# Kernel tuning notes

Hardware: AMD Instinct MI355X
Metric: run time of the kernel (lower is better)

## Reference

```python
import jax, jax.numpy as jnp
import numpy as np

N = 50000        # n_nodes
E = 1_600_000    # n_edges (avg degree 32)
D = 128          # in_feat_dim
H = 128          # hidden_dim
OUT = 128        # out_feat_dim
EDGE_IN = 2 * D + 1 + 1  # h[row], h[col], dist_sq, edge_attr
act = jax.nn.silu


def _lin(k, fan_in, fan_out):
    lim = 1.0 / np.sqrt(fan_in)
    return jax.random.uniform(k, (fan_in, fan_out), jnp.float32, -lim, lim)


def setup_inputs() -> dict:
    key = jax.random.key(0)
    ks = jax.random.split(key, 24)
    inp = {
        "h": jax.random.normal(ks[0], (N, D), jnp.float32),
        "x": jax.random.normal(ks[1], (N, 3), jnp.float32),
        "edge_attr": jax.random.normal(ks[2], (E, 1), jnp.float32),
        "v_init": jax.random.normal(ks[3], (N, 3), jnp.float32),
        "edge_index": jax.random.randint(ks[4], (2, E), 0, N, jnp.int32),
        # edge_mlp: Linear(258,H), act, Linear(H,H), act
        "edge_W1": _lin(ks[5], EDGE_IN, H), "edge_b1": jnp.zeros((H,), jnp.float32),
        "edge_W2": _lin(ks[6], H, H), "edge_b2": jnp.zeros((H,), jnp.float32),
        # coord_mlp: Linear(H,H), act, Linear(H,1,bias=False)
        "coord_W1": _lin(ks[7], H, H), "coord_b1": jnp.zeros((H,), jnp.float32),
        "coord_W2": _lin(ks[8], H, 1),
        # infer_edge_step: Linear(H,H//2), act, Linear(H//2,1), sigmoid
        "inf_W1": _lin(ks[9], H, H // 2), "inf_b1": jnp.zeros((H // 2,), jnp.float32),
        "inf_W2": _lin(ks[10], H // 2, 1), "inf_b2": jnp.zeros((1,), jnp.float32),
        # node_mlp: Linear(D+H,H), act, Linear(H,OUT)
        "node_W1": _lin(ks[11], D + H, H), "node_b1": jnp.zeros((H,), jnp.float32),
        "node_W2": _lin(ks[12], H, OUT), "node_b2": jnp.zeros((OUT,), jnp.float32),
        # momentum_vel_mlp: Linear(D,H), act, Linear(H,1,bias=False)
        "vel_W1": _lin(ks[13], D, H), "vel_b1": jnp.zeros((H,), jnp.float32),
        "vel_W2": _lin(ks[14], H, 1),
    }
    return inp


def reference(h, x, edge_attr, v_init, edge_index,
              edge_W1, edge_b1, edge_W2, edge_b2,
              coord_W1, coord_b1, coord_W2,
              inf_W1, inf_b1, inf_W2, inf_b2,
              node_W1, node_b1, node_W2, node_b2,
              vel_W1, vel_b1, vel_W2):
    row, col = edge_index[0], edge_index[1]
    x_diff = x[row] - x[col]                                   # [E,3]
    dist_sq = jnp.sum(x_diff * x_diff, axis=1, keepdims=True)  # [E,1]
    ef = jnp.concatenate([h[row], h[col], dist_sq, edge_attr], axis=1)  # [E,258]
    m_ij = act(act(ef @ edge_W1 + edge_b1) @ edge_W2 + edge_b2)        # [E,H]
    e_ij = jax.nn.sigmoid(act(m_ij @ inf_W1 + inf_b1) @ inf_W2 + inf_b2)  # [E,1]
    phi_x = act(m_ij @ coord_W1 + coord_b1) @ coord_W2                 # [E,1]
    x_update = e_ij * (phi_x * x_diff)                                 # [E,3]
    m_ij = e_ij * m_ij

    vel_scale = act(h @ vel_W1 + vel_b1) @ vel_W2                      # [N,1]
    v_out = v_init * vel_scale                                         # [N,3]

    agg_x = jax.ops.segment_sum(x_update, row, num_segments=N)         # [N,3]
    m_i = jax.ops.segment_sum(m_ij, row, num_segments=N)               # [N,H]
    deg = jax.ops.segment_sum(jnp.ones((E,), jnp.float32), row, num_segments=N)
    has_edge = (deg > 0)[:, None]
    # nodes with no outgoing edges keep their original x (original loop skips them)
    x_out = jnp.where(has_edge, x + v_out + agg_x / (N - 1), x)

    node_in = jnp.concatenate([h, m_i], axis=1)                        # [N,D+H]
    h_out = act(node_in @ node_W1 + node_b1) @ node_W2 + node_b2       # [N,OUT]
    return (h_out, x_out, v_out)
```

## Files before the change

kernel.cpp:

```cpp
#include <hip/hip_runtime.h>
#include <hip/hip_bf16.h>

typedef __attribute__((ext_vector_type(8))) short short8;
typedef __attribute__((ext_vector_type(4))) float f32x4;
typedef __hip_bfloat16 bf16;

__device__ __forceinline__ short f2bs_rn(float f) {
    unsigned u = __builtin_bit_cast(unsigned, f);
    u += 0x7FFF + ((u >> 16) & 1);
    return (short)(u >> 16);
}
__device__ __forceinline__ float bs2f(short s) {
    unsigned u = ((unsigned)(unsigned short)s) << 16;
    return __builtin_bit_cast(float, u);
}
__device__ __forceinline__ float ldf(const void* p, int i, int flag) {
    return flag ? bs2f(((const short*)p)[i]) : ((const float*)p)[i];
}
__device__ __forceinline__ short ldbits(const void* p, int i, int flag) {
    return flag ? ((const short*)p)[i] : f2bs_rn(((const float*)p)[i]);
}
__device__ __forceinline__ void stf(void* p, int i, float v, int flag) {
    if (flag) ((bf16*)p)[i] = __float2bfloat16(v);
    else ((float*)p)[i] = v;
}
__device__ __forceinline__ float nz(float v) { return (v == v) ? v : 0.f; }
__device__ __forceinline__ float siluf(float v) {
    return v * __builtin_amdgcn_rcpf(1.f + __expf(-v));
}
__device__ __forceinline__ float sigmf(float v) {
    return __builtin_amdgcn_rcpf(1.f + __expf(-v));
}

__global__ void detect_kernel(const unsigned int* __restrict__ hw, int* __restrict__ flag) {
    unsigned int w = hw[threadIdx.x];
    unsigned int e = (w >> 7) & 0xFF;
    bool ok = (e >= 113 && e <= 135);
    unsigned long long m = __ballot(ok);
    if (threadIdx.x == 0) *flag = (__popcll(m) >= 32) ? 1 : 0;
}

__global__ void prep_kernel(
    const void* eW1, const void* eW2, const void* cW1, const void* iW1,
    const void* eb1, const void* eb2, const void* cb1, const void* cw2,
    const void* ib1, const void* iw2, const void* ib2, const void* nb1,
    const void* nb2, const void* vb1, const void* vW2,
    const void* nW1, const void* nW2, const void* vW1,
    short* __restrict__ W1t, short* __restrict__ W2t,
    short* __restrict__ cW1t, short* __restrict__ iW1t,
    float* __restrict__ biasblk, short* __restrict__ nW1b,
    short* __restrict__ nW2b, short* __restrict__ vW1b,
    const int* __restrict__ flagp) {
    const int flag = *flagp;
    int i = blockIdx.x * 256 + threadIdx.x;
    if (i < 36864) {
        int c = i >> 9, r = i & 511;
        int kc = c >> 3, nt = c & 7;
        int ln = r >> 3, j = r & 7;
        int k = kc * 32 + ((ln >> 4) << 3) + j;
        int n = nt * 16 + (ln & 15);
        W1t[i] = (k < 258) ? ldbits(eW1, k * 128 + n, flag) : (short)0;
        return;
    }
    i -= 36864;
    if (i < 16384) {
        int c = i >> 9, r = i & 511;
        int kc = c >> 3, nt = c & 7;
        int ln = r >> 3, j = r & 7;
        int k = kc * 32 + ((ln >> 4) << 3) + j;
        int n = nt * 16 + (ln & 15);
        W2t[i] = ldbits(eW2, k * 128 + n, flag);
        return;
    }
    i -= 16384;
    if (i < 16384) {
        int c = i >> 9, r = i & 511;
        int kc = c >> 3, nt = c & 7;
        int ln = r >> 3, j = r & 7;
        int k = kc * 32 + ((ln >> 4) << 3) + j;
        int n = nt * 16 + (ln & 15);
        cW1t[i] = ldbits(cW1, k * 128 + n, flag);
        return;
    }
    i -= 16384;
    if (i < 8192) {
        int c = i >> 9, r = i & 511;
        int kc = c >> 2, nt = c & 3;
        int ln = r >> 3, j = r & 7;
        int k = kc * 32 + ((ln >> 4) << 3) + j;
        int n = nt * 16 + (ln & 15);
        iW1t[i] = ldbits(iW1, k * 64 + n, flag);
        return;
    }
    i -= 8192;
    if (i < 1412) {
        float v;
        if (i < 128) v = ldf(eb1, i, flag);
        else if (i < 256) v = ldf(eb2, i - 128, flag);
        else if (i < 384) v = ldf(cb1, i - 256, flag);
        else if (i < 512) v = ldf(cw2, i - 384, flag);
        else if (i < 576) v = ldf(ib1, i - 512, flag);
        else if (i < 640) v = ldf(iw2, i - 576, flag);
        else if (i < 644) v = (i == 640) ? ldf(ib2, 0, flag) : 0.f;
        else if (i < 772) v = ldf(nb1, i - 644, flag);
        else if (i < 900) v = ldf(nb2, i - 772, flag);
        else if (i < 1028) v = ldf(vb1, i - 900, flag);
        else if (i < 1156) v = ldf(vW2, i - 1028, flag);
        else if (i < 1284) v = ldf(eW1, 256 * 128 + (i - 1156), flag);
        else v = ldf(eW1, 257 * 128 + (i - 1284), flag);
        biasblk[i] = v;
        return;
    }
    i -= 1412;
    if (i < 32768) {
        int c = i >> 9, r = i & 511;
        int kc = c >> 3, nt = c & 7;
        int ln = r >> 3, j = r & 7;
        int k = kc * 32 + ((ln >> 4) << 3) + j;
        int n = nt * 16 + (ln & 15);
        nW1b[i] = ldbits(nW1, k * 128 + n, flag);
        return;
    }
    i -= 32768;
    if (i < 16384) {
        int c = i >> 9, r = i & 511;
        int kc = c >> 3, nt = c & 7;
        int ln = r >> 3, j = r & 7;
        int k = kc * 32 + ((ln >> 4) << 3) + j;
        int n = nt * 16 + (ln & 15);
        nW2b[i] = ldbits(nW2, k * 128 + n, flag);
        return;
    }
    i -= 16384;
    if (i < 16384) {
        int c = i >> 9, r = i & 511;
        int kc = c >> 3, nt = c & 7;
        int ln = r >> 3, j = r & 7;
        int k = kc * 32 + ((ln >> 4) << 3) + j;
        int n = nt * 16 + (ln & 15);
        vW1b[i] = ldbits(vW1, k * 128 + n, flag);
    }
}

__global__ void convh_kernel(const void* __restrict__ h, short* __restrict__ hb,
                             const int* __restrict__ flagp, int n) {
    const int flag = *flagp;
    int i = blockIdx.x * 256 + threadIdx.x;
    if (i < n) hb[i] = ldbits(h, i, flag);
}

__global__ __launch_bounds__(256) void hw1_kernel(
    const short* __restrict__ hb, const short* __restrict__ W1t,
    short* __restrict__ hA, short* __restrict__ hB, int N) {
    const int tid = threadIdx.x;
    const int wv = tid >> 6;
    const int lane = tid & 63;
    const int n15 = lane & 15;
    const int quad = lane >> 4;
    const int base = blockIdx.x * 128 + wv * 32;

    f32x4 accA[2][8], accB[2][8];
#pragma unroll
    for (int m = 0; m < 2; ++m)
#pragma unroll
        for (int nt = 0; nt < 8; ++nt) {
            accA[m][nt] = (f32x4){0.f, 0.f, 0.f, 0.f};
            accB[m][nt] = (f32x4){0.f, 0.f, 0.f, 0.f};
        }

#pragma unroll
    for (int kc = 0; kc < 4; ++kc) {
        short8 a[2];
#pragma unroll
        for (int m = 0; m < 2; ++m) {
            int node = base + m * 16 + n15;
            if (node >= N) node = N - 1;
            a[m] = *(const short8*)(hb + node * 128 + kc * 32 + quad * 8);
        }
        const short* bpA = W1t + (kc * 8) * 512 + lane * 8;
        const short* bpB = W1t + ((kc + 4) * 8) * 512 + lane * 8;
#pragma unroll
        for (int nt = 0; nt < 8; ++nt) {
            short8 ba = *(const short8*)(bpA + nt * 512);
            short8 bb = *(const short8*)(bpB + nt * 512);
            accA[0][nt] = __builtin_amdgcn_mfma_f32_16x16x32_bf16(a[0], ba, accA[0][nt], 0, 0, 0);
            accA[1][nt] = __builtin_amdgcn_mfma_f32_16x16x32_bf16(a[1], ba, accA[1][nt], 0, 0, 0);
            accB[0][nt] = __builtin_amdgcn_mfma_f32_16x16x32_bf16(a[0], bb, accB[0][nt], 0, 0, 0);
            accB[1][nt] = __builtin_amdgcn_mfma_f32_16x16x32_bf16(a[1], bb, accB[1][nt], 0, 0, 0);
        }
    }

#pragma unroll
    for (int m = 0; m < 2; ++m)
#pragma unroll
        for (int nt = 0; nt < 8; ++nt)
#pragma unroll
            for (int r = 0; r < 4; ++r) {
                int node = base + m * 16 + quad * 4 + r;
                if (node < N) {
                    hA[node * 128 + nt * 16 + n15] = f2bs_rn(accA[m][nt][r]);
                    hB[node * 128 + nt * 16 + n15] = f2bs_rn(accB[m][nt][r]);
                }
            }
}

__global__ void count_kernel(const int* __restrict__ erow, int* __restrict__ cnt, int E) {
    int i = blockIdx.x * 256 + threadIdx.x;
    if (i < E) atomicAdd(&cnt[erow[i]], 1);
}

__global__ __launch_bounds__(1024) void scan1_kernel(const int* __restrict__ cnt,
                                                     int* __restrict__ off,
                                                     int* __restrict__ bsum, int N) {
    __shared__ int sm[1024];
    int t = threadIdx.x, i = blockIdx.x * 1024 + t;
    int c = (i < N) ? cnt[i] : 0;
    sm[t] = c;
    __syncthreads();
    for (int d = 1; d < 1024; d <<= 1) {
        int v = (t >= d) ? sm[t - d] : 0;
        __syncthreads();
        sm[t] += v;
        __syncthreads();
    }
    if (i < N) off[i] = sm[t] - c;
    if (t == 1023) bsum[blockIdx.x] = sm[1023];
}
__global__ void scan2_kernel(const int* __restrict__ bsum, int* __restrict__ bpre, int nb) {
    if (threadIdx.x == 0) {
        int run = 0;
        for (int b = 0; b < nb; ++b) { bpre[b] = run; run += bsum[b]; }
    }
}
__global__ void scan3_kernel(int* __restrict__ off, const int* __restrict__ bpre, int N) {
    int i = blockIdx.x * 256 + threadIdx.x;
    if (i < N) off[i] += bpre[i >> 10];
}
__global__ void fill_kernel(const int* __restrict__ erow, const int* __restrict__ off,
                            int* __restrict__ cur, int* __restrict__ elist, int E) {
    int i = blockIdx.x * 256 + threadIdx.x;
    if (i < E) {
        int r = erow[i];
        int p = off[r] + atomicAdd(&cur[r], 1);
        elist[p] = i;
    }
}

template <bool CSR>
__global__ __launch_bounds__(256, 6) void edge_kernel(
    const short* __restrict__ hA, const short* __restrict__ hB,
    const void* __restrict__ x, const void* __restrict__ eattr,
    const int* __restrict__ erow, const int* __restrict__ ecol,
    const int* __restrict__ elist,
    const short* __restrict__ W2f, const short* __restrict__ cW1f,
    const short* __restrict__ iW1f,
    const float* __restrict__ biasblk,
    float* __restrict__ m_i, float* __restrict__ agg_x, int E,
    const int* __restrict__ flagp) {
    const int flag = *flagp;
    __shared__ __align__(16) short tiles[4][16 * 136];
    const float* b1f = biasblk;
    const float* b2f = biasblk + 128;
    const float* cb1f = biasblk + 256;
    const float* cw2f = biasblk + 384;
    const float* ib1f = biasblk + 512;
    const float* iw2f = biasblk + 576;
    const float ib2s = biasblk[640];
    const float* w1df = biasblk + 1156;
    const float* w1af = biasblk + 1284;

    int bid;
    {
        const int nwg = gridDim.x;
        const int qq = nwg >> 3, r8 = nwg & 7;
        const int xcd = blockIdx.x & 7, idx = blockIdx.x >> 3;
        const int base = (xcd < r8) ? xcd * (qq + 1) : r8 * (qq + 1) + (xcd - r8) * qq;
        bid = base + idx;
    }

    const int tid = threadIdx.x;
    const int wv = tid >> 6;
    const int lane = tid & 63;
    const int n15 = lane & 15;
    const int quad = lane >> 4;
    const int wb = bid * 64 + wv * 16;

    int row_e, col_e;
    float dist, attr;
    {
        int slot = wb + n15;
        int sL = (slot < E) ? slot : (E - 1);
        int eL = CSR ? elist[sL] : sL;
        row_e = erow[eL];
        col_e = ecol[eL];
        float d = 0.f;
#pragma unroll
        for (int dd = 0; dd < 3; ++dd) {
            float xd = ldf(x, row_e * 3 + dd, flag) - ldf(x, col_e * 3 + dd, flag);
            d += xd * xd;
        }
        dist = d;
        attr = ldf(eattr, eL, flag);
    }

    short8 cB[4];
#pragma unroll
    for (int c = 0; c < 4; ++c)
        cB[c] = *(const short8*)(hB + col_e * 128 + c * 32 + quad * 8);

    short* tl = tiles[wv];
    short8 h1[4];
#pragma unroll
    for (int c = 0; c < 4; ++c) {
        short8 ra = *(const short8*)(hA + row_e * 128 + c * 32 + quad * 8);
        short8 ov;
#pragma unroll
        for (int j = 0; j < 8; ++j) {
            int f = c * 32 + quad * 8 + j;
            float v = bs2f(ra[j]) + bs2f(cB[c][j])
                    + dist * w1df[f] + attr * w1af[f] + b1f[f];
            ov[j] = f2bs_rn(siluf(v));
        }
        h1[c] = ov;
    }

    f32x4 acc2[8];
#pragma unroll
    for (int nt = 0; nt < 8; ++nt) acc2[nt] = (f32x4){0.f, 0.f, 0.f, 0.f};
#pragma unroll
    for (int kc = 0; kc < 4; ++kc) {
        short8 a = h1[kc];
        const short* bp = W2f + (kc * 8) * 512 + lane * 8;
#pragma unroll
        for (int nt = 0; nt < 8; ++nt) {
            short8 b = *(const short8*)(bp + nt * 512);
            acc2[nt] = __builtin_amdgcn_mfma_f32_16x16x32_bf16(a, b, acc2[nt], 0, 0, 0);
        }
    }

#pragma unroll
    for (int nt = 0; nt < 8; ++nt) {
        float bv = b2f[nt * 16 + n15];
#pragma unroll
        for (int r = 0; r < 4; ++r)
            tl[(quad * 4 + r) * 136 + nt * 16 + n15] = f2bs_rn(siluf(acc2[nt][r] + bv));
    }

    f32x4 acc4[4];
#pragma unroll
    for (int nt = 0; nt < 4; ++nt) acc4[nt] = (f32x4){0.f, 0.f, 0.f, 0.f};
#pragma unroll
    for (int kc = 0; kc < 4; ++kc) {
        short8 a = *(const short8*)(tl + n15 * 136 + kc * 32 + quad * 8);
        const short* bp = iW1f + (kc * 4) * 512 + lane * 8;
#pragma unroll
        for (int nt = 0; nt < 4; ++nt) {
            short8 b = *(const short8*)(bp + nt * 512);
            acc4[nt] = __builtin_amdgcn_mfma_f32_16x16x32_bf16(a, b, acc4[nt], 0, 0, 0);
        }
    }
    float eij[4];
    {
        float inp[4] = {0.f, 0.f, 0.f, 0.f};
#pragma unroll
        for (int nt = 0; nt < 4; ++nt) {
            float ib = ib1f[nt * 16 + n15];
            float iw = iw2f[nt * 16 + n15];
#pragma unroll
            for (int r = 0; r < 4; ++r) inp[r] += siluf(acc4[nt][r] + ib) * iw;
        }
#pragma unroll
        for (int mk = 1; mk < 16; mk <<= 1)
#pragma unroll
            for (int r = 0; r < 4; ++r) inp[r] += __shfl_xor(inp[r], mk);
#pragma unroll
        for (int r = 0; r < 4; ++r) eij[r] = sigmf(inp[r] + ib2s);
    }

    f32x4 acc3[8];
#pragma unroll
    for (int nt = 0; nt < 8; ++nt) acc3[nt] = (f32x4){0.f, 0.f, 0.f, 0.f};
#pragma unroll
    for (int kc = 0; kc < 4; ++kc) {
        short8 a = *(const short8*)(tl + n15 * 136 + kc * 32 + quad * 8);
        const short* bp = cW1f + (kc * 8) * 512 + lane * 8;
#pragma unroll
        for (int nt = 0; nt < 8; ++nt) {
            short8 b = *(const short8*)(bp + nt * 512);
            acc3[nt] = __builtin_amdgcn_mfma_f32_16x16x32_bf16(a, b, acc3[nt], 0, 0, 0);
        }
    }

    {
        float php[4] = {0.f, 0.f, 0.f, 0.f};
#pragma unroll
        for (int nt = 0; nt < 8; ++nt) {
            float cb = cb1f[nt * 16 + n15];
            float cw = cw2f[nt * 16 + n15];
#pragma unroll
            for (int r = 0; r < 4; ++r) php[r] += siluf(acc3[nt][r] + cb) * cw;
        }
#pragma unroll
        for (int mk = 1; mk < 16; mk <<= 1)
#pragma unroll
            for (int r = 0; r < 4; ++r) php[r] += __shfl_xor(php[r], mk);

        float sv[4];
#pragma unroll
        for (int r = 0; r < 4; ++r) sv[r] = eij[r] * php[r];
        const int srcl = (n15 >> 2) * 16;
        float t0 = __shfl(sv[0], srcl);
        float t1 = __shfl(sv[1], srcl);
        float t2 = __shfl(sv[2], srcl);
        float t3 = __shfl(sv[3], srcl);
        const int rr = n15 & 3;
        float s_e = (rr == 0) ? t0 : (rr == 1) ? t1 : (rr == 2) ? t2 : t3;

        float val = 0.f;
        if (quad < 3) {
            float xd = ldf(x, row_e * 3 + quad, flag) - ldf(x, col_e * 3 + quad, flag);
            val = ((wb + n15) < E) ? nz(s_e * xd) : 0.f;
        }

        const int ebase = wb;
        if (CSR) {
            int p = 0;
            while (p < 16 && (ebase + p) < E) {
                int rowp = __shfl(row_e, p);
                unsigned bal = (unsigned)__ballot(row_e == rowp) & 0xFFFFu;
                unsigned bits = (~bal) >> p;
                int q = p + __builtin_ctz(bits);

                float av = (n15 >= p && n15 < q) ? val : 0.f;
#pragma unroll
                for (int mk = 1; mk < 16; mk <<= 1) av += __shfl_xor(av, mk);
                if (n15 == 0 && quad < 3) atomicAdd(&agg_x[rowp * 3 + quad], av);

                float s[8];
#pragma unroll
                for (int nt = 0; nt < 8; ++nt) s[nt] = 0.f;
#pragma unroll
                for (int r = 0; r < 4; ++r) {
                    int idx = quad * 4 + r;
                    bool in = (idx >= p) && (idx < q) && ((ebase + idx) < E);
                    float w = in ? eij[r] : 0.f;
#pragma unroll
                    for (int nt = 0; nt < 8; ++nt)
                        s[nt] += w * bs2f(tl[idx * 136 + nt * 16 + n15]);
                }
#pragma unroll
                for (int nt = 0; nt < 8; ++nt) {
                    s[nt] += __shfl_xor(s[nt], 16);
                    s[nt] += __shfl_xor(s[nt], 32);
                }
                if (quad == 0) {
#pragma unroll
                    for (int nt = 0; nt < 8; ++nt)
                        atomicAdd(&m_i[(size_t)rowp * 128 + nt * 16 + n15], nz(s[nt]));
                }
                p = q;
            }
        } else {
            if (quad < 3 && (wb + n15) < E)
                atomicAdd(&agg_x[row_e * 3 + quad], val);
#pragma unroll
            for (int nt = 0; nt < 8; ++nt)
#pragma unroll
                for (int r = 0; r < 4; ++r) {
                    int idx = quad * 4 + r;
                    if ((ebase + idx) < E) {
                        int er = __shfl(row_e, idx);
                        atomicAdd(&m_i[er * 128 + nt * 16 + n15],
                                  nz(eij[r] * bs2f(tl[idx * 136 + nt * 16 + n15])));
                    }
                }
        }
    }
}

__global__ __launch_bounds__(256, 4) void node_kernel(
    const short* __restrict__ hb, const void* __restrict__ x,
    const void* __restrict__ v_init,
    const int* __restrict__ cnt,
    const float* __restrict__ m_i, const float* __restrict__ agg_x,
    const short* __restrict__ nW1f, const short* __restrict__ nW2f,
    const short* __restrict__ vW1f, const float* __restrict__ biasblk,
    void* __restrict__ out, int N, int xbase, int vbase, float inv_nm1,
    const int* __restrict__ flagp) {
    const int flag = *flagp;
    __shared__ __align__(16) short tiles[4][16 * 136];
    const float* nb1f = biasblk + 644;
    const float* nb2f = biasblk + 772;
    const float* vb1f = biasblk + 900;
    const float* vW2f = biasblk + 1028;

    const int tid = threadIdx.x;
    const int wv = tid >> 6;
    const int lane = tid & 63;
    const int n15 = lane & 15;
    const int quad = lane >> 4;
    const int base = blockIdx.x * 64 + wv * 16;

    short* tl = tiles[wv];

    {
        int node = base + n15;
        if (node >= N) node = N - 1;
#pragma unroll
        for (int c = 0; c < 4; ++c) {
            const float* mp = m_i + (size_t)node * 128 + c * 32 + quad * 8;
            short8 ov;
#pragma unroll
            for (int j = 0; j < 8; ++j) ov[j] = f2bs_rn(nz(mp[j]));
            *(short8*)(tl + n15 * 136 + c * 32 + quad * 8) = ov;
        }
    }
    int anode = base + n15;
    if (anode >= N) anode = N - 1;

    f32x4 acc[8];
#pragma unroll
    for (int nt = 0; nt < 8; ++nt) acc[nt] = (f32x4){0.f, 0.f, 0.f, 0.f};
#pragma unroll
    for (int kc = 0; kc < 4; ++kc) {
        short8 a = *(const short8*)(hb + (size_t)anode * 128 + kc * 32 + quad * 8);
        const short* bp = vW1f + (kc * 8) * 512 + lane * 8;
#pragma unroll
        for (int nt = 0; nt < 8; ++nt) {
            short8 b = *(const short8*)(bp + nt * 512);
            acc[nt] = __builtin_amdgcn_mfma_f32_16x16x32_bf16(a, b, acc[nt], 0, 0, 0);
        }
    }
    float vsc[4] = {0.f, 0.f, 0.f, 0.f};
#pragma unroll
    for (int nt = 0; nt < 8; ++nt) {
        int j = nt * 16 + n15;
        float vb = vb1f[j];
        float vw = vW2f[j];
#pragma unroll
        for (int r = 0; r < 4; ++r) vsc[r] += siluf(acc[nt][r] + vb) * vw;
    }
#pragma unroll
    for (int mk = 1; mk < 16; mk <<= 1)
#pragma unroll
        for (int r = 0; r < 4; ++r) vsc[r] += __shfl_xor(vsc[r], mk);

#pragma unroll
    for (int nt = 0; nt < 8; ++nt) acc[nt] = (f32x4){0.f, 0.f, 0.f, 0.f};
#pragma unroll
    for (int kc = 0; kc < 8; ++kc) {
        short8 a;
        if (kc < 4) a = *(const short8*)(hb + (size_t)anode * 128 + kc * 32 + quad * 8);
        else        a = *(const short8*)(tl + n15 * 136 + (kc - 4) * 32 + quad * 8);
        const short* bp = nW1f + (kc * 8) * 512 + lane * 8;
#pragma unroll
        for (int nt = 0; nt < 8; ++nt) {
            short8 b = *(const short8*)(bp + nt * 512);
            acc[nt] = __builtin_amdgcn_mfma_f32_16x16x32_bf16(a, b, acc[nt], 0, 0, 0);
        }
    }
#pragma unroll
    for (int nt = 0; nt < 8; ++nt) {
        float bv = nb1f[nt * 16 + n15];
#pragma unroll
        for (int r = 0; r < 4; ++r)
            tl[(quad * 4 + r) * 136 + nt * 16 + n15] = f2bs_rn(siluf(acc[nt][r] + bv));
    }

#pragma unroll
    for (int nt = 0; nt < 8; ++nt) acc[nt] = (f32x4){0.f, 0.f, 0.f, 0.f};
#pragma unroll
    for (int kc = 0; kc < 4; ++kc) {
        short8 a = *(const short8*)(tl + n15 * 136 + kc * 32 + quad * 8);
        const short* bp = nW2f + (kc * 8) * 512 + lane * 8;
#pragma unroll
        for (int nt = 0; nt < 8; ++nt) {
            short8 b = *(const short8*)(bp + nt * 512);
            acc[nt] = __builtin_amdgcn_mfma_f32_16x16x32_bf16(a, b, acc[nt], 0, 0, 0);
        }
    }
#pragma unroll
    for (int nt = 0; nt < 8; ++nt) {
        float bv = nb2f[nt * 16 + n15];
#pragma unroll
        for (int r = 0; r < 4; ++r) {
            int node = base + quad * 4 + r;
            if (node < N) stf(out, node * 128 + nt * 16 + n15, nz(acc[nt][r] + bv), flag);
        }
    }

    if (n15 < 3) {
#pragma unroll
        for (int r = 0; r < 4; ++r) {
            int node = base + quad * 4 + r;
            if (node >= N) continue;
            int d = n15;
            float vj = nz(ldf(v_init, node * 3 + d, flag) * vsc[r]);
            stf(out, vbase + node * 3 + d, vj, flag);
            float xv = ldf(x, node * 3 + d, flag);
            float xo = (cnt[node] > 0) ? xv + vj + nz(agg_x[node * 3 + d]) * inv_nm1 : xv;
            stf(out, xbase + node * 3 + d, nz(xo), flag);
        }
    }
}

template <bool CSR>
__global__ __launch_bounds__(256, 2) void edge_kernel_old(
    const short* __restrict__ hb, const void* __restrict__ x,
    const void* __restrict__ eattr,
    const int* __restrict__ erow, const int* __restrict__ ecol,
    const int* __restrict__ elist,
    const short* __restrict__ W1f, const short* __restrict__ W2f,
    const short* __restrict__ cW1f, const short* __restrict__ iW1f,
    const float* __restrict__ biasblk,
    float* __restrict__ m_i, float* __restrict__ agg_x, int E,
    const int* __restrict__ flagp) {
    const int flag = *flagp;
    __shared__ __align__(16) short tiles[8][16 * 136];
    const float* b1f = biasblk;
    const float* b2f = biasblk + 128;
    const float* cb1f = biasblk + 256;
    const float* cw2f = biasblk + 384;
    const float* ib1f = biasblk + 512;
    const float* iw2f = biasblk + 576;
    const float ib2s = biasblk[640];

    const int tid = threadIdx.x;
    const int wv = tid >> 6;
    const int lane = tid & 63;
    const int n15 = lane & 15;
    const int quad = lane >> 4;
    const int wb = blockIdx.x * 128 + wv * 32;

    int row_e[2], col_e[2];
    float dist[2], attr[2];
#pragma unroll
    for (int m = 0; m < 2; ++m) {
        int slot = wb + m * 16 + n15;
        int sL = (slot < E) ? slot : (E - 1);
        int eL = CSR ? elist[sL] : sL;
        row_e[m] = erow[eL];
        col_e[m] = ecol[eL];
        float d = 0.f;
#pragma unroll
        for (int dd = 0; dd < 3; ++dd) {
            float xd = ldf(x, row_e[m] * 3 + dd, flag) - ldf(x, col_e[m] * 3 + dd, flag);
            d += xd * xd;
        }
        dist[m] = d;
        attr[m] = ldf(eattr, eL, flag);
    }

    short8 cA[2][4];
#pragma unroll
    for (int m = 0; m < 2; ++m)
#pragma unroll
        for (int c = 0; c < 4; ++c)
            cA[m][c] = *(const short8*)(hb + col_e[m] * 128 + c * 32 + quad * 8);

    f32x4 acc1[2][8];
#pragma unroll
    for (int m = 0; m < 2; ++m)
#pragma unroll
        for (int nt = 0; nt < 8; ++nt) acc1[m][nt] = (f32x4){0.f, 0.f, 0.f, 0.f};

#pragma unroll
    for (int kc = 0; kc < 9; ++kc) {
        short8 a[2];
        if (kc < 4) {
            a[0] = *(const short8*)(hb + row_e[0] * 128 + kc * 32 + quad * 8);
            a[1] = *(const short8*)(hb + row_e[1] * 128 + kc * 32 + quad * 8);
        } else if (kc < 8) {
            a[0] = cA[0][kc - 4];
            a[1] = cA[1][kc - 4];
        } else {
#pragma unroll
            for (int m = 0; m < 2; ++m) {
#pragma unroll
                for (int t = 0; t < 8; ++t) a[m][t] = 0;
                if (quad == 0) { a[m][0] = f2bs_rn(dist[m]); a[m][1] = f2bs_rn(attr[m]); }
            }
        }
        const short* bp = W1f + (kc * 8) * 512 + lane * 8;
#pragma unroll
        for (int nt = 0; nt < 8; ++nt) {
            short8 b = *(const short8*)(bp + nt * 512);
            acc1[0][nt] = __builtin_amdgcn_mfma_f32_16x16x32_bf16(a[0], b, acc1[0][nt], 0, 0, 0);
            acc1[1][nt] = __builtin_amdgcn_mfma_f32_16x16x32_bf16(a[1], b, acc1[1][nt], 0, 0, 0);
        }
    }

#pragma unroll
    for (int m = 0; m < 2; ++m) {
        short* tl = tiles[wv * 2 + m];
#pragma unroll
        for (int nt = 0; nt < 8; ++nt) {
            float bv = b1f[nt * 16 + n15];
#pragma unroll
            for (int r = 0; r < 4; ++r)
                tl[(quad * 4 + r) * 136 + nt * 16 + n15] = f2bs_rn(siluf(acc1[m][nt][r] + bv));
        }
    }

    f32x4 acc2[2][8];
#pragma unroll
    for (int m = 0; m < 2; ++m)
#pragma unroll
        for (int nt = 0; nt < 8; ++nt) acc2[m][nt] = (f32x4){0.f, 0.f, 0.f, 0.f};
#pragma unroll
    for (int kc = 0; kc < 4; ++kc) {
        short8 a[2];
#pragma unroll
        for (int m = 0; m < 2; ++m)
            a[m] = *(const short8*)(tiles[wv * 2 + m] + n15 * 136 + kc * 32 + quad * 8);
        const short* bp = W2f + (kc * 8) * 512 + lane * 8;
#pragma unroll
        for (int nt = 0; nt < 8; ++nt) {
            short8 b = *(const short8*)(bp + nt * 512);
            acc2[0][nt] = __builtin_amdgcn_mfma_f32_16x16x32_bf16(a[0], b, acc2[0][nt], 0, 0, 0);
            acc2[1][nt] = __builtin_amdgcn_mfma_f32_16x16x32_bf16(a[1], b, acc2[1][nt], 0, 0, 0);
        }
    }

    float mv[2][8][4];
#pragma unroll
    for (int m = 0; m < 2; ++m) {
        short* tl = tiles[wv * 2 + m];
#pragma unroll
        for (int nt = 0; nt < 8; ++nt) {
            float bv = b2f[nt * 16 + n15];
#pragma unroll
            for (int r = 0; r < 4; ++r) {
                float v = siluf(acc2[m][nt][r] + bv);
                mv[m][nt][r] = v;
                tl[(quad * 4 + r) * 136 + nt * 16 + n15] = f2bs_rn(v);
            }
        }
    }

    f32x4 acc4[2][4];
#pragma unroll
    for (int m = 0; m < 2; ++m)
#pragma unroll
        for (int nt = 0; nt < 4; ++nt) acc4[m][nt] = (f32x4){0.f, 0.f, 0.f, 0.f};
#pragma unroll
    for (int kc = 0; kc < 4; ++kc) {
        short8 a[2];
#pragma unroll
        for (int m = 0; m < 2; ++m)
            a[m] = *(const short8*)(tiles[wv * 2 + m] + n15 * 136 + kc * 32 + quad * 8);
        const short* bp = iW1f + (kc * 4) * 512 + lane * 8;
#pragma unroll
        for (int nt = 0; nt < 4; ++nt) {
            short8 b = *(const short8*)(bp + nt * 512);
            acc4[0][nt] = __builtin_amdgcn_mfma_f32_16x16x32_bf16(a[0], b, acc4[0][nt], 0, 0, 0);
            acc4[1][nt] = __builtin_amdgcn_mfma_f32_16x16x32_bf16(a[1], b, acc4[1][nt], 0, 0, 0);
        }
    }
    float eij[2][4];
#pragma unroll
    for (int m = 0; m < 2; ++m) {
        float inp[4] = {0.f, 0.f, 0.f, 0.f};
#pragma unroll
        for (int nt = 0; nt < 4; ++nt) {
            float ib = ib1f[nt * 16 + n15];
            float iw = iw2f[nt * 16 + n15];
#pragma unroll
            for (int r = 0; r < 4; ++r) inp[r] += siluf(acc4[m][nt][r] + ib) * iw;
        }
#pragma unroll
        for (int mk = 1; mk < 16; mk <<= 1)
#pragma unroll
            for (int r = 0; r < 4; ++r) inp[r] += __shfl_xor(inp[r], mk);
#pragma unroll
        for (int r = 0; r < 4; ++r) eij[m][r] = sigmf(inp[r] + ib2s);
    }

    f32x4 acc3[2][8];
#pragma unroll
    for (int m = 0; m < 2; ++m)
#pragma unroll
        for (int nt = 0; nt < 8; ++nt) acc3[m][nt] = (f32x4){0.f, 0.f, 0.f, 0.f};
#pragma unroll
    for (int kc = 0; kc < 4; ++kc) {
        short8 a[2];
#pragma unroll
        for (int m = 0; m < 2; ++m)
            a[m] = *(const short8*)(tiles[wv * 2 + m] + n15 * 136 + kc * 32 + quad * 8);
        const short* bp = cW1f + (kc * 8) * 512 + lane * 8;
#pragma unroll
        for (int nt = 0; nt < 8; ++nt) {
            short8 b = *(const short8*)(bp + nt * 512);
            acc3[0][nt] = __builtin_amdgcn_mfma_f32_16x16x32_bf16(a[0], b, acc3[0][nt], 0, 0, 0);
            acc3[1][nt] = __builtin_amdgcn_mfma_f32_16x16x32_bf16(a[1], b, acc3[1][nt], 0, 0, 0);
        }
    }

#pragma unroll
    for (int m = 0; m < 2; ++m) {
        float php[4] = {0.f, 0.f, 0.f, 0.f};
#pragma unroll
        for (int nt = 0; nt < 8; ++nt) {
            float cb = cb1f[nt * 16 + n15];
            float cw = cw2f[nt * 16 + n15];
#pragma unroll
            for (int r = 0; r < 4; ++r) php[r] += siluf(acc3[m][nt][r] + cb) * cw;
        }
#pragma unroll
        for (int mk = 1; mk < 16; mk <<= 1)
#pragma unroll
            for (int r = 0; r < 4; ++r) php[r] += __shfl_xor(php[r], mk);

        const int ebase = wb + m * 16;
        int er[4], ec[4];
        bool mk4[4];
#pragma unroll
        for (int r = 0; r < 4; ++r) {
            er[r] = __shfl(row_e[m], quad * 4 + r);
            ec[r] = __shfl(col_e[m], quad * 4 + r);
            mk4[r] = (ebase + quad * 4 + r) < E;
        }

        if (n15 == 0) {
#pragma unroll
            for (int r = 0; r < 4; ++r) {
                if (!mk4[r]) continue;
                float s = eij[m][r] * php[r];
#pragma unroll
                for (int d = 0; d < 3; ++d) {
                    float xd = ldf(x, er[r] * 3 + d, flag) - ldf(x, ec[r] * 3 + d, flag);
                    atomicAdd(&agg_x[er[r] * 3 + d], nz(s * xd));
                }
            }
        }

        if (CSR) {
            int p = 0;
            while (p < 16 && (ebase + p) < E) {
                int rowp = __shfl(row_e[m], p);
                unsigned bal = (unsigned)__ballot(row_e[m] == rowp) & 0xFFFFu;
                unsigned bits = (~bal) >> p;
                int q = p + __builtin_ctz(bits);
                float s[8];
#pragma unroll
                for (int nt = 0; nt < 8; ++nt) s[nt] = 0.f;
#pragma unroll
                for (int r = 0; r < 4; ++r) {
                    int idx = quad * 4 + r;
                    bool in = (idx >= p) && (idx < q) && ((ebase + idx) < E);
                    float w = in ? eij[m][r] : 0.f;
#pragma unroll
                    for (int nt = 0; nt < 8; ++nt) s[nt] += w * mv[m][nt][r];
                }
#pragma unroll
                for (int nt = 0; nt < 8; ++nt) {
                    s[nt] += __shfl_xor(s[nt], 16);
                    s[nt] += __shfl_xor(s[nt], 32);
                }
                if (quad == 0) {
#pragma unroll
                    for (int nt = 0; nt < 8; ++nt)
                        atomicAdd(&m_i[(size_t)rowp * 128 + nt * 16 + n15], nz(s[nt]));
                }
                p = q;
            }
        } else {
#pragma unroll
            for (int nt = 0; nt < 8; ++nt)
#pragma unroll
                for (int r = 0; r < 4; ++r)
                    if (mk4[r]) atomicAdd(&m_i[er[r] * 128 + nt * 16 + n15],
                                          nz(eij[m][r] * mv[m][nt][r]));
        }
    }
}

extern "C" void kernel_launch(void* const* d_in, const int* in_sizes, int n_in,
                              void* d_out, int out_size, void* d_ws, size_t ws_size,
                              hipStream_t stream) {
    const void* h = d_in[0];
    const void* x = d_in[1];
    const void* eattr = d_in[2];
    const void* v_init = d_in[3];
    const int* eidx = (const int*)d_in[4];

    const int N = in_sizes[0] / 128;
    const int E = in_sizes[4] / 2;
    const int* erow = eidx;
    const int* ecol = eidx + E;

    char* ws = (char*)d_ws;
    int* flag = (int*)ws;
    short* W1t = (short*)(ws + 256);
    short* W2t = (short*)(ws + 73984);
    short* cW1t = (short*)(ws + 106752);
    short* iW1t = (short*)(ws + 139520);
    float* biasblk = (float*)(ws + 155904);
    short* nW1b = (short*)(ws + 162048);
    short* nW2b = (short*)(ws + 227584);
    short* vW1b = (short*)(ws + 260352);
    int* bsum = (int*)(ws + 293120);
    int* bpre = (int*)(ws + 293632);
    short* hb = (short*)(ws + 294144);
    size_t o = 294144 + (size_t)N * 256;
    size_t oZero = o;
    int* cnt = (int*)(ws + o); o += (size_t)N * 4;
    int* cur = (int*)(ws + o); o += (size_t)N * 4;
    float* agg_x = (float*)(ws + o); o += (size_t)N * 12;
    float* m_i = (float*)(ws + o); o += (size_t)N * 512;
    size_t zeroBytes = o - oZero;
    int* offp = (int*)(ws + o); o += (size_t)(N + 16) * 4;
    int* elist = (int*)(ws + o); o += (size_t)E * 4;
    const size_t need_csr = o;
    short* hA = (short*)(ws + o); o += (size_t)N * 256;
    short* hB = (short*)(ws + o); o += (size_t)N * 256;
    const size_t need_full = o;

    const bool csr = (ws_size >= need_csr);
    const bool pre = (ws_size >= need_full);

    detect_kernel<<<1, 64, 0, stream>>>((const unsigned int*)h, flag);

    const int prep_elems = 36864 + 16384 + 16384 + 8192 + 1412 + 32768 + 16384 + 16384;
    prep_kernel<<<(prep_elems + 255) / 256, 256, 0, stream>>>(
        d_in[5], d_in[7], d_in[9], d_in[12],
        d_in[6], d_in[8], d_in[10], d_in[11], d_in[13], d_in[14], d_in[15],
        d_in[17], d_in[19], d_in[21], d_in[22],
        d_in[16], d_in[18], d_in[20],
        W1t, W2t, cW1t, iW1t, biasblk, nW1b, nW2b, vW1b, flag);

    convh_kernel<<<(N * 128 + 255) / 256, 256, 0, stream>>>(h, hb, flag, N * 128);

    if (pre) {
        hw1_kernel<<<(N + 127) / 128, 256, 0, stream>>>(hb, W1t, hA, hB, N);
    }

    hipMemsetAsync((void*)(ws + oZero), 0, zeroBytes, stream);
    count_kernel<<<(E + 255) / 256, 256, 0, stream>>>(erow, cnt, E);

    if (csr) {
        const int nb = (N + 1023) / 1024;
        scan1_kernel<<<nb, 1024, 0, stream>>>(cnt, offp, bsum, N);
        scan2_kernel<<<1, 64, 0, stream>>>(bsum, bpre, nb);
        scan3_kernel<<<(N + 255) / 256, 256, 0, stream>>>(offp, bpre, N);
        fill_kernel<<<(E + 255) / 256, 256, 0, stream>>>(erow, offp, cur, elist, E);
    }

    if (pre && csr) {
        edge_kernel<true><<<(E + 63) / 64, 256, 0, stream>>>(
            hA, hB, x, eattr, erow, ecol, elist, W2t, cW1t, iW1t, biasblk,
            m_i, agg_x, E, flag);
    } else if (csr) {
        edge_kernel_old<true><<<(E + 127) / 128, 256, 0, stream>>>(
            hb, x, eattr, erow, ecol, elist, W1t, W2t, cW1t, iW1t, biasblk,
            m_i, agg_x, E, flag);
    } else {
        edge_kernel_old<false><<<(E + 127) / 128, 256, 0, stream>>>(
            hb, x, eattr, erow, ecol, nullptr, W1t, W2t, cW1t, iW1t, biasblk,
            m_i, agg_x, E, flag);
    }

    node_kernel<<<(N + 63) / 64, 256, 0, stream>>>(
        hb, x, v_init, cnt, m_i, agg_x,
        nW1b, nW2b, vW1b, biasblk, d_out, N, N * 128, N * 131,
        1.0f / (float)(N - 1), flag);
}
```

Measured before the change: 971.9 us.

## Fuse h conversion with degree counting, parallelize block scan, tweak edge occupancy

Merges the bf16 conversion of h with the per-row edge-count atomics into one launch, and moves the zeroing memset earlier so the counts start from zero. The serial single-thread scan of block sums becomes a 1024-thread shared-memory scan. The hw1 precompute launch is moved after the CSR build, and edge_kernel's launch-bounds occupancy hint drops from 6 to 5 blocks per CU. These aim to cut launch overhead and serial work, and the occupancy hint trades waves for more registers per thread.

```diff
diff --git a/kernel.cpp b/kernel.cpp
--- a/kernel.cpp
+++ b/kernel.cpp
@@ -142,11 +142,13 @@
     }
 }
 
-__global__ void convh_kernel(const void* __restrict__ h, short* __restrict__ hb,
-                             const int* __restrict__ flagp, int n) {
+__global__ void convh_count_kernel(const void* __restrict__ h, short* __restrict__ hb,
+                                   const int* __restrict__ erow, int* __restrict__ cnt,
+                                   const int* __restrict__ flagp, int n, int E) {
     const int flag = *flagp;
     int i = blockIdx.x * 256 + threadIdx.x;
     if (i < n) hb[i] = ldbits(h, i, flag);
+    if (i < E) atomicAdd(&cnt[erow[i]], 1);
 }
 
 __global__ __launch_bounds__(256) void hw1_kernel(
@@ -202,11 +204,6 @@
                     hB[node * 128 + nt * 16 + n15] = f2bs_rn(accB[m][nt][r]);
                 }
             }
-}
-
-__global__ void count_kernel(const int* __restrict__ erow, int* __restrict__ cnt, int E) {
-    int i = blockIdx.x * 256 + threadIdx.x;
-    if (i < E) atomicAdd(&cnt[erow[i]], 1);
 }
 
 __global__ __launch_bounds__(1024) void scan1_kernel(const int* __restrict__ cnt,
@@ -226,11 +223,20 @@
     if (i < N) off[i] = sm[t] - c;
     if (t == 1023) bsum[blockIdx.x] = sm[1023];
 }
-__global__ void scan2_kernel(const int* __restrict__ bsum, int* __restrict__ bpre, int nb) {
-    if (threadIdx.x == 0) {
-        int run = 0;
-        for (int b = 0; b < nb; ++b) { bpre[b] = run; run += bsum[b]; }
-    }
+__global__ __launch_bounds__(1024) void scan2_kernel(const int* __restrict__ bsum,
+                                                     int* __restrict__ bpre, int nb) {
+    __shared__ int sm[1024];
+    int t = threadIdx.x;
+    int c = (t < nb) ? bsum[t] : 0;
+    sm[t] = c;
+    __syncthreads();
+    for (int d = 1; d < 1024; d <<= 1) {
+        int v = (t >= d) ? sm[t - d] : 0;
+        __syncthreads();
+        sm[t] += v;
+        __syncthreads();
+    }
+    if (t < nb) bpre[t] = sm[t] - c;
 }
 __global__ void scan3_kernel(int* __restrict__ off, const int* __restrict__ bpre, int N) {
     int i = blockIdx.x * 256 + threadIdx.x;
@@ -247,7 +253,7 @@
 }
 
 template <bool CSR>
-__global__ __launch_bounds__(256, 6) void edge_kernel(
+__global__ __launch_bounds__(256, 5) void edge_kernel(
     const short* __restrict__ hA, const short* __restrict__ hB,
     const void* __restrict__ x, const void* __restrict__ eattr,
     const int* __restrict__ erow, const int* __restrict__ ecol,
@@ -921,6 +927,8 @@
 
     detect_kernel<<<1, 64, 0, stream>>>((const unsigned int*)h, flag);
 
+    hipMemsetAsync((void*)(ws + oZero), 0, zeroBytes, stream);
+
     const int prep_elems = 36864 + 16384 + 16384 + 8192 + 1412 + 32768 + 16384 + 16384;
     prep_kernel<<<(prep_elems + 255) / 256, 256, 0, stream>>>(
         d_in[5], d_in[7], d_in[9], d_in[12],
@@ -929,21 +937,22 @@
         d_in[16], d_in[18], d_in[20],
         W1t, W2t, cW1t, iW1t, biasblk, nW1b, nW2b, vW1b, flag);
 
-    convh_kernel<<<(N * 128 + 255) / 256, 256, 0, stream>>>(h, hb, flag, N * 128);
-
-    if (pre) {
-        hw1_kernel<<<(N + 127) / 128, 256, 0, stream>>>(hb, W1t, hA, hB, N);
-    }
-
-    hipMemsetAsync((void*)(ws + oZero), 0, zeroBytes, stream);
-    count_kernel<<<(E + 255) / 256, 256, 0, stream>>>(erow, cnt, E);
+    {
+        int total = (N * 128 > E) ? N * 128 : E;
+        convh_count_kernel<<<(total + 255) / 256, 256, 0, stream>>>(
+            h, hb, erow, cnt, flag, N * 128, E);
+    }
 
     if (csr) {
         const int nb = (N + 1023) / 1024;
         scan1_kernel<<<nb, 1024, 0, stream>>>(cnt, offp, bsum, N);
-        scan2_kernel<<<1, 64, 0, stream>>>(bsum, bpre, nb);
+        scan2_kernel<<<1, 1024, 0, stream>>>(bsum, bpre, nb);
         scan3_kernel<<<(N + 255) / 256, 256, 0, stream>>>(offp, bpre, N);
         fill_kernel<<<(E + 255) / 256, 256, 0, stream>>>(erow, offp, cur, elist, E);
+    }
+
+    if (pre) {
+        hw1_kernel<<<(N + 127) / 128, 256, 0, stream>>>(hb, W1t, hA, hB, N);
     }
 
     if (pre && csr) {
```

New measurement: 1.058 ms. +8.8%, slower.
